# Kernel optimization log

Measured on AMD Instinct MI355X. Metric: run time of the kernel, lower is better.

Reference implementation:

```python
import jax, jax.numpy as jnp
import numpy as np
from jax import lax

NUM_KP = 17
MAX_PEOPLE = 30
HEAT_THRESH = 0.1
STRIDE = 4  # heatmap -> image coordinate scale

def setup_inputs() -> dict:
    key = jax.random.key(0)
    heatmaps = jax.random.uniform(key, (32, NUM_KP, 256, 256), dtype=jnp.float32)
    return {"heatmaps": heatmaps}

def reference(heatmaps):
    # heatmaps: [B, C, H, W]
    B, C, H, W = heatmaps.shape
    neg_inf = jnp.float32(-jnp.inf)
    # 3x3 max-pool NMS (stride 1, pad 1) batched over all B*C channels at once.
    hmax = lax.reduce_window(
        heatmaps, neg_inf, lax.max,
        window_dimensions=(1, 1, 3, 3),
        window_strides=(1, 1, 1, 1),
        padding=((0, 0), (0, 0), (1, 1), (1, 1)),
    )
    nms = heatmaps * (hmax == heatmaps).astype(heatmaps.dtype)
    # Threshold + descending sort + take top max_people, done as a batched top_k.
    flat = nms.reshape(B, C, H * W)
    masked = jnp.where(flat > HEAT_THRESH, flat, neg_inf)
    scores, idx = lax.top_k(masked, MAX_PEOPLE)          # [B, C, max_people]
    y = idx // W
    x = idx % W
    coords = jnp.stack([x, y], axis=-1).astype(jnp.int32) * STRIDE  # [B,C,max_people,2] as (x,y)*4
    valid = scores > HEAT_THRESH                          # padding mask (original output is ragged)
    return coords, scores, valid
```

## Files before the change

kernel.cpp:

```cpp
#include <hip/hip_runtime.h>
#include <stdint.h>

#define NUM_KP 17
#define BATCH  32
#define HDIM   256
#define WDIM   256
#define NCH    (BATCH * NUM_KP)
#define MAXP   30
#define QBLKS  4
#define K1THREADS 256
#define SEGCAP 640

#define NBINS  4096
#define QB     125953

#define WS_REQUIRED ((size_t)NCH * QBLKS * MAXP * 8)

__device__ __forceinline__ unsigned long long shfl_down_u64(unsigned long long v, int off) {
    unsigned lo = (unsigned)v, hi = (unsigned)(v >> 32);
    lo = __shfl_down(lo, off);
    hi = __shfl_down(hi, off);
    return ((unsigned long long)hi << 32) | lo;
}
__device__ __forceinline__ unsigned long long shfl_u64(unsigned long long v, int lane) {
    unsigned lo = (unsigned)v, hi = (unsigned)(v >> 32);
    lo = __shfl(lo, lane);
    hi = __shfl(hi, lane);
    return ((unsigned long long)hi << 32) | lo;
}
__device__ __forceinline__ unsigned quant12(float v) {
    int b = (int)(__float_as_uint(v) >> 13) - QB;
    b = b < 1 ? 1 : (b > NBINS - 1 ? NBINS - 1 : b);
    return (unsigned)b;
}

__global__ __launch_bounds__(K1THREADS, 7)
void pose_part_kernel(const float* __restrict__ heat, unsigned long long* __restrict__ part) {
    __shared__ unsigned s_buf[4 * SEGCAP];
    __shared__ unsigned s_hist[NBINS / 2];
    __shared__ int s_gsum[256];
    __shared__ unsigned long long s_ref[256];
    __shared__ int s_wcnt[4];
    __shared__ int s_nref, s_tau;

    const int tid  = threadIdx.x;
    const int chan = blockIdx.x >> 2;
    const int qtr  = blockIdx.x & 3;
    const int wave = tid >> 6;
    const int lane = tid & 63;
    const float NEGINF = -__builtin_inff();
    const float* __restrict__ cp = heat + (size_t)chan * (HDIM * WDIM);

    for (int i = tid; i < NBINS / 2; i += K1THREADS) s_hist[i] = 0;
    if (tid == 0) s_nref = 0;
    __syncthreads();

    const int r0 = (qtr << 6) + (wave << 4);
    const float* colp = cp + (lane << 2);
    const float4 NEG4 = make_float4(NEGINF, NEGINF, NEGINF, NEGINF);
    const unsigned long long ltmask = (1ull << lane) - 1ull;
    unsigned* __restrict__ seg = s_buf + wave * SEGCAP;
    int wavecnt = 0;

    auto LD = [&](int r) -> float4 {
        return (r >= 0 && r < HDIM) ? *(const float4*)(colp + (r << 8)) : NEG4;
    };
    auto push = [&](float v, int pidx, int pos) {
        if (pos < SEGCAP) {
            unsigned q = quant12(v);
            seg[pos] = (q << 16) | (unsigned)pidx;
            atomicAdd(&s_hist[q >> 1], 1u << ((q & 1) << 4));
        }
    };
    auto process = [&](const float4& up, const float4& md, const float4& dn, int r) {
        float vm0 = fmaxf(up.x, fmaxf(md.x, dn.x));
        float vm1 = fmaxf(up.y, fmaxf(md.y, dn.y));
        float vm2 = fmaxf(up.z, fmaxf(md.z, dn.z));
        float vm3 = fmaxf(up.w, fmaxf(md.w, dn.w));
        float left  = __shfl_up(vm3, 1);   if (lane == 0)  left  = NEGINF;
        float right = __shfl_down(vm0, 1); if (lane == 63) right = NEGINF;
        float h0 = fmaxf(left, fmaxf(vm0, vm1));
        float h1 = fmaxf(vm0, fmaxf(vm1, vm2));
        float h2 = fmaxf(vm1, fmaxf(vm2, vm3));
        float h3 = fmaxf(vm2, fmaxf(vm3, right));

        bool p0 = md.x > 0.1f && md.x == h0;
        bool p1 = md.y > 0.1f && md.y == h1;
        bool p2 = md.z > 0.1f && md.z == h2;
        bool p3 = md.w > 0.1f && md.w == h3;
        unsigned long long b0 = __ballot(p0), b1 = __ballot(p1);
        unsigned long long b2 = __ballot(p2), b3 = __ballot(p3);
        int c0 = __popcll(b0), c1 = __popcll(b1), c2 = __popcll(b2);
        int before = wavecnt;
        wavecnt += c0 + c1 + c2 + __popcll(b3);

        const int base = (r << 8) | (lane << 2);
        if (p0) push(md.x, base + 0, before + __popcll(b0 & ltmask));
        if (p1) push(md.y, base + 1, before + c0 + __popcll(b1 & ltmask));
        if (p2) push(md.z, base + 2, before + c0 + c1 + __popcll(b2 & ltmask));
        if (p3) push(md.w, base + 3, before + c0 + c1 + c2 + __popcll(b3 & ltmask));
    };

    float4 rm   = LD(r0 - 1);
    float4 cur0 = LD(r0 + 0), cur1 = LD(r0 + 1), cur2 = LD(r0 + 2), cur3 = LD(r0 + 3);
    #pragma unroll
    for (int g = 0; g < 4; ++g) {
        const int rb = r0 + (g << 2);
        float4 n0, n1, n2, n3;
        if (g < 3) { n0 = LD(rb + 4); n1 = LD(rb + 5); n2 = LD(rb + 6); n3 = LD(rb + 7); }
        else       { n0 = LD(rb + 4); n1 = NEG4; n2 = NEG4; n3 = NEG4; }
        process(rm,   cur0, cur1, rb + 0);
        process(cur0, cur1, cur2, rb + 1);
        process(cur1, cur2, cur3, rb + 2);
        process(cur2, cur3, n0,   rb + 3);
        rm = cur3; cur0 = n0; cur1 = n1; cur2 = n2; cur3 = n3;
    }
    if (lane == 0) s_wcnt[wave] = wavecnt < SEGCAP ? wavecnt : SEGCAP;
    __syncthreads();

    {
        int s = 0;
        #pragma unroll
        for (int j = 0; j < 8; ++j) {
            unsigned w = s_hist[tid * 8 + j];
            s += (int)(w & 0xFFFFu) + (int)(w >> 16);
        }
        s_gsum[tid] = s;
    }
    __syncthreads();
    if (wave == 0) {
        int u0 = s_gsum[(lane << 2) + 0], u1 = s_gsum[(lane << 2) + 1];
        int u2 = s_gsum[(lane << 2) + 2], u3 = s_gsum[(lane << 2) + 3];
        int t = u0 + u1 + u2 + u3;
        int R = t;
        #pragma unroll
        for (int off = 1; off < 64; off <<= 1) {
            int v = __shfl_down(R, off);
            if (lane + off < 64) R += v;
        }
        int E = R - t;
        int sg3 = u3 + E, sg2 = u2 + sg3, sg1 = u1 + sg2, sg0 = u0 + sg1;
        unsigned long long mask = __ballot(sg0 >= MAXP);
        if (mask == 0ull) {
            if (lane == 0) s_tau = 0;
        } else {
            int hi = 63 - __builtin_clzll(mask);
            if (lane == hi) {
                int k, above;
                if      (sg3 >= MAXP) { k = 3; above = E;   }
                else if (sg2 >= MAXP) { k = 2; above = sg3; }
                else if (sg1 >= MAXP) { k = 1; above = sg2; }
                else                  { k = 0; above = sg1; }
                int g = (lane << 2) + k;
                int cum = above, tau = 0;
                for (int b = (g << 4) + 15; b >= (g << 4); --b) {
                    cum += (int)((s_hist[b >> 1] >> ((b & 1) << 4)) & 0xFFFFu);
                    if (cum >= MAXP) { tau = b; break; }
                }
                s_tau = tau;
            }
        }
    }
    __syncthreads();

    const unsigned tau = (unsigned)s_tau;
    for (int s = 0; s < 4; ++s) {
        const int c = s_wcnt[s];
        const unsigned* sb = s_buf + s * SEGCAP;
        for (int i = tid; i < c; i += K1THREADS) {
            unsigned p = sb[i];
            if ((p >> 16) >= tau) {
                int pos = atomicAdd(&s_nref, 1);
                if (pos < 256) {
                    unsigned idx = p & 0xFFFFu;
                    float sc = cp[idx];
                    s_ref[pos] = ((unsigned long long)__float_as_uint(sc) << 32) | (unsigned)(~idx);
                }
            }
        }
    }
    __syncthreads();
    const int nref = s_nref < 256 ? s_nref : 256;

    if (tid < 64) {
        unsigned long long* pk = part + (size_t)blockIdx.x * MAXP;
        unsigned long long k0 = (tid       < nref) ? s_ref[tid]       : 0ull;
        unsigned long long k1 = (tid + 64  < nref) ? s_ref[tid + 64]  : 0ull;
        unsigned long long k2 = (tid + 128 < nref) ? s_ref[tid + 128] : 0ull;
        unsigned long long k3 = (tid + 192 < nref) ? s_ref[tid + 192] : 0ull;
        for (int r = 0; r < MAXP; ++r) {
            unsigned long long best = k0; int bs = 0;
            if (k1 > best) { best = k1; bs = 1; }
            if (k2 > best) { best = k2; bs = 2; }
            if (k3 > best) { best = k3; bs = 3; }
            unsigned long long key = best;
            int slot = (bs << 6) | tid;
            #pragma unroll
            for (int off = 32; off > 0; off >>= 1) {
                unsigned long long ok = shfl_down_u64(key, off);
                int os = __shfl_down(slot, off);
                if (ok > key) { key = ok; slot = os; }
            }
            key  = shfl_u64(key, 0);
            slot = __shfl(slot, 0);
            if ((slot & 63) == tid) {
                int which = slot >> 6;
                if      (which == 0) k0 = 0ull;
                else if (which == 1) k1 = 0ull;
                else if (which == 2) k2 = 0ull;
                else                 k3 = 0ull;
            }
            if (tid == 0) pk[r] = key;
        }
    }
}

__global__ __launch_bounds__(64)
void pose_merge_kernel(const unsigned long long* __restrict__ part,
                       float* __restrict__ out, int out_size) {
    const int chan = blockIdx.x;
    const int lane = threadIdx.x;
    const float NEGINF = -__builtin_inff();
    const unsigned long long* pk = part + (size_t)chan * (QBLKS * MAXP);

    unsigned long long k0 = pk[lane];
    unsigned long long k1 = (lane + 64 < QBLKS * MAXP) ? pk[lane + 64] : 0ull;

    for (int r = 0; r < MAXP; ++r) {
        unsigned long long best = k0; int bs = 0;
        if (k1 > best) { best = k1; bs = 1; }
        unsigned long long key = best;
        int slot = (bs << 6) | lane;
        #pragma unroll
        for (int off = 32; off > 0; off >>= 1) {
            unsigned long long ok = shfl_down_u64(key, off);
            int os = __shfl_down(slot, off);
            if (ok > key) { key = ok; slot = os; }
        }
        key  = shfl_u64(key, 0);
        slot = __shfl(slot, 0);
        if ((slot & 63) == lane) {
            if ((slot >> 6) == 0) k0 = 0ull; else k1 = 0ull;
        }
        if (lane == 0) {
            float sc, vld; unsigned idx;
            if (key != 0ull) {
                sc  = __uint_as_float((unsigned)(key >> 32));
                idx = (~(unsigned)key) & 0xFFFFu;
                vld = 1.0f;
            } else { sc = NEGINF; idx = 0u; vld = 0.0f; }
            int x = (int)(idx & 255), y = (int)(idx >> 8);
            long long cb = ((long long)chan * MAXP + r) * 2;
            if (cb + 1 < out_size) {
                out[cb]     = (float)(x * 4);
                out[cb + 1] = (float)(y * 4);
            }
            long long so = (long long)NCH * MAXP * 2 + (long long)chan * MAXP + r;
            if (so < out_size) out[so] = sc;
            long long vo = (long long)NCH * MAXP * 3 + (long long)chan * MAXP + r;
            if (vo < out_size) out[vo] = vld;
        }
    }
}

extern "C" void kernel_launch(void* const* d_in, const int* in_sizes, int n_in,
                              void* d_out, int out_size, void* d_ws, size_t ws_size,
                              hipStream_t stream) {
    const float* heat = (const float*)d_in[0];
    float* out = (float*)d_out;
    unsigned long long* part = (unsigned long long*)d_ws;
    hipLaunchKernelGGL(pose_part_kernel, dim3(NCH * QBLKS), dim3(K1THREADS), 0, stream,
                       heat, part);
    hipLaunchKernelGGL(pose_merge_kernel, dim3(NCH), dim3(64), 0, stream,
                       part, out, out_size);
}
```

Baseline: 237.6 us.

## Recompute NMS sweep instead of buffering candidates; rank-based top-k selection

Drops the per-wave shared-memory candidate buffer and instead re-runs the 3x3 NMS sweep a second time, emitting only candidates whose quantized score meets the threshold bin. This frees shared memory, so launch bounds are raised to eight blocks per SM. The serial 30-round wave-shuffle argmax in both kernels is replaced by parallel rank counting over shared memory, and the merge kernel uses 128 threads. The cost is a second read of the heatmap tile (likely served from cache) and the NMS arithmetic done twice.

Result: slower. 394.2 us (+65.9%).

```diff
diff --git a/kernel.cpp b/kernel.cpp
--- a/kernel.cpp
+++ b/kernel.cpp
@@ -9,38 +9,23 @@
 #define MAXP   30
 #define QBLKS  4
 #define K1THREADS 256
-#define SEGCAP 640
 
 #define NBINS  4096
 #define QB     125953
 
 #define WS_REQUIRED ((size_t)NCH * QBLKS * MAXP * 8)
 
-__device__ __forceinline__ unsigned long long shfl_down_u64(unsigned long long v, int off) {
-    unsigned lo = (unsigned)v, hi = (unsigned)(v >> 32);
-    lo = __shfl_down(lo, off);
-    hi = __shfl_down(hi, off);
-    return ((unsigned long long)hi << 32) | lo;
-}
-__device__ __forceinline__ unsigned long long shfl_u64(unsigned long long v, int lane) {
-    unsigned lo = (unsigned)v, hi = (unsigned)(v >> 32);
-    lo = __shfl(lo, lane);
-    hi = __shfl(hi, lane);
-    return ((unsigned long long)hi << 32) | lo;
-}
 __device__ __forceinline__ unsigned quant12(float v) {
     int b = (int)(__float_as_uint(v) >> 13) - QB;
     b = b < 1 ? 1 : (b > NBINS - 1 ? NBINS - 1 : b);
     return (unsigned)b;
 }
 
-__global__ __launch_bounds__(K1THREADS, 7)
+__global__ __launch_bounds__(K1THREADS, 8)
 void pose_part_kernel(const float* __restrict__ heat, unsigned long long* __restrict__ part) {
-    __shared__ unsigned s_buf[4 * SEGCAP];
     __shared__ unsigned s_hist[NBINS / 2];
     __shared__ int s_gsum[256];
     __shared__ unsigned long long s_ref[256];
-    __shared__ int s_wcnt[4];
     __shared__ int s_nref, s_tau;
 
     const int tid  = threadIdx.x;
@@ -58,21 +43,12 @@
     const int r0 = (qtr << 6) + (wave << 4);
     const float* colp = cp + (lane << 2);
     const float4 NEG4 = make_float4(NEGINF, NEGINF, NEGINF, NEGINF);
-    const unsigned long long ltmask = (1ull << lane) - 1ull;
-    unsigned* __restrict__ seg = s_buf + wave * SEGCAP;
-    int wavecnt = 0;
 
     auto LD = [&](int r) -> float4 {
         return (r >= 0 && r < HDIM) ? *(const float4*)(colp + (r << 8)) : NEG4;
     };
-    auto push = [&](float v, int pidx, int pos) {
-        if (pos < SEGCAP) {
-            unsigned q = quant12(v);
-            seg[pos] = (q << 16) | (unsigned)pidx;
-            atomicAdd(&s_hist[q >> 1], 1u << ((q & 1) << 4));
-        }
-    };
-    auto process = [&](const float4& up, const float4& md, const float4& dn, int r) {
+    auto process = [&](const float4& up, const float4& md, const float4& dn, int r,
+                       auto&& emit) {
         float vm0 = fmaxf(up.x, fmaxf(md.x, dn.x));
         float vm1 = fmaxf(up.y, fmaxf(md.y, dn.y));
         float vm2 = fmaxf(up.z, fmaxf(md.z, dn.z));
@@ -83,39 +59,34 @@
         float h1 = fmaxf(vm0, fmaxf(vm1, vm2));
         float h2 = fmaxf(vm1, fmaxf(vm2, vm3));
         float h3 = fmaxf(vm2, fmaxf(vm3, right));
-
-        bool p0 = md.x > 0.1f && md.x == h0;
-        bool p1 = md.y > 0.1f && md.y == h1;
-        bool p2 = md.z > 0.1f && md.z == h2;
-        bool p3 = md.w > 0.1f && md.w == h3;
-        unsigned long long b0 = __ballot(p0), b1 = __ballot(p1);
-        unsigned long long b2 = __ballot(p2), b3 = __ballot(p3);
-        int c0 = __popcll(b0), c1 = __popcll(b1), c2 = __popcll(b2);
-        int before = wavecnt;
-        wavecnt += c0 + c1 + c2 + __popcll(b3);
-
         const int base = (r << 8) | (lane << 2);
-        if (p0) push(md.x, base + 0, before + __popcll(b0 & ltmask));
-        if (p1) push(md.y, base + 1, before + c0 + __popcll(b1 & ltmask));
-        if (p2) push(md.z, base + 2, before + c0 + c1 + __popcll(b2 & ltmask));
-        if (p3) push(md.w, base + 3, before + c0 + c1 + c2 + __popcll(b3 & ltmask));
+        if (md.x > 0.1f && md.x == h0) emit(md.x, base + 0);
+        if (md.y > 0.1f && md.y == h1) emit(md.y, base + 1);
+        if (md.z > 0.1f && md.z == h2) emit(md.z, base + 2);
+        if (md.w > 0.1f && md.w == h3) emit(md.w, base + 3);
     };
-
-    float4 rm   = LD(r0 - 1);
-    float4 cur0 = LD(r0 + 0), cur1 = LD(r0 + 1), cur2 = LD(r0 + 2), cur3 = LD(r0 + 3);
-    #pragma unroll
-    for (int g = 0; g < 4; ++g) {
-        const int rb = r0 + (g << 2);
-        float4 n0, n1, n2, n3;
-        if (g < 3) { n0 = LD(rb + 4); n1 = LD(rb + 5); n2 = LD(rb + 6); n3 = LD(rb + 7); }
-        else       { n0 = LD(rb + 4); n1 = NEG4; n2 = NEG4; n3 = NEG4; }
-        process(rm,   cur0, cur1, rb + 0);
-        process(cur0, cur1, cur2, rb + 1);
-        process(cur1, cur2, cur3, rb + 2);
-        process(cur2, cur3, n0,   rb + 3);
-        rm = cur3; cur0 = n0; cur1 = n1; cur2 = n2; cur3 = n3;
-    }
-    if (lane == 0) s_wcnt[wave] = wavecnt < SEGCAP ? wavecnt : SEGCAP;
+    auto sweep = [&](auto&& emit) {
+        float4 rm   = LD(r0 - 1);
+        float4 cur0 = LD(r0 + 0), cur1 = LD(r0 + 1), cur2 = LD(r0 + 2), cur3 = LD(r0 + 3);
+        #pragma unroll
+        for (int g = 0; g < 4; ++g) {
+            const int rb = r0 + (g << 2);
+            float4 n0, n1, n2, n3;
+            if (g < 3) { n0 = LD(rb + 4); n1 = LD(rb + 5); n2 = LD(rb + 6); n3 = LD(rb + 7); }
+            else       { n0 = LD(rb + 4); n1 = NEG4; n2 = NEG4; n3 = NEG4; }
+            process(rm,   cur0, cur1, rb + 0, emit);
+            process(cur0, cur1, cur2, rb + 1, emit);
+            process(cur1, cur2, cur3, rb + 2, emit);
+            process(cur2, cur3, n0,   rb + 3, emit);
+            rm = cur3; cur0 = n0; cur1 = n1; cur2 = n2; cur3 = n3;
+        }
+    };
+
+    sweep([&](float v, int pidx) {
+        unsigned q = quant12(v);
+        atomicAdd(&s_hist[q >> 1], 1u << ((q & 1) << 4));
+        (void)pidx;
+    });
     __syncthreads();
 
     {
@@ -164,100 +135,65 @@
     __syncthreads();
 
     const unsigned tau = (unsigned)s_tau;
-    for (int s = 0; s < 4; ++s) {
-        const int c = s_wcnt[s];
-        const unsigned* sb = s_buf + s * SEGCAP;
-        for (int i = tid; i < c; i += K1THREADS) {
-            unsigned p = sb[i];
-            if ((p >> 16) >= tau) {
-                int pos = atomicAdd(&s_nref, 1);
-                if (pos < 256) {
-                    unsigned idx = p & 0xFFFFu;
-                    float sc = cp[idx];
-                    s_ref[pos] = ((unsigned long long)__float_as_uint(sc) << 32) | (unsigned)(~idx);
-                }
+    sweep([&](float v, int pidx) {
+        if (quant12(v) >= tau) {
+            int pos = atomicAdd(&s_nref, 1);
+            if (pos < 256) {
+                s_ref[pos] = ((unsigned long long)__float_as_uint(v) << 32)
+                           | (unsigned)(~(unsigned)pidx);
             }
         }
-    }
-    __syncthreads();
+    });
+    __syncthreads();
+
     const int nref = s_nref < 256 ? s_nref : 256;
-
-    if (tid < 64) {
-        unsigned long long* pk = part + (size_t)blockIdx.x * MAXP;
-        unsigned long long k0 = (tid       < nref) ? s_ref[tid]       : 0ull;
-        unsigned long long k1 = (tid + 64  < nref) ? s_ref[tid + 64]  : 0ull;
-        unsigned long long k2 = (tid + 128 < nref) ? s_ref[tid + 128] : 0ull;
-        unsigned long long k3 = (tid + 192 < nref) ? s_ref[tid + 192] : 0ull;
-        for (int r = 0; r < MAXP; ++r) {
-            unsigned long long best = k0; int bs = 0;
-            if (k1 > best) { best = k1; bs = 1; }
-            if (k2 > best) { best = k2; bs = 2; }
-            if (k3 > best) { best = k3; bs = 3; }
-            unsigned long long key = best;
-            int slot = (bs << 6) | tid;
-            #pragma unroll
-            for (int off = 32; off > 0; off >>= 1) {
-                unsigned long long ok = shfl_down_u64(key, off);
-                int os = __shfl_down(slot, off);
-                if (ok > key) { key = ok; slot = os; }
-            }
-            key  = shfl_u64(key, 0);
-            slot = __shfl(slot, 0);
-            if ((slot & 63) == tid) {
-                int which = slot >> 6;
-                if      (which == 0) k0 = 0ull;
-                else if (which == 1) k1 = 0ull;
-                else if (which == 2) k2 = 0ull;
-                else                 k3 = 0ull;
-            }
-            if (tid == 0) pk[r] = key;
-        }
-    }
-}
-
-__global__ __launch_bounds__(64)
+    unsigned long long* pk = part + (size_t)blockIdx.x * MAXP;
+    const int nv = nref < MAXP ? nref : MAXP;
+    if (tid >= nv && tid < MAXP) pk[tid] = 0ull;
+    if (tid < nref) {
+        unsigned long long k = s_ref[tid];
+        int rank = 0;
+        for (int j = 0; j < nref; ++j) rank += (s_ref[j] > k) ? 1 : 0;
+        if (rank < MAXP) pk[rank] = k;
+    }
+}
+
+__global__ __launch_bounds__(128)
 void pose_merge_kernel(const unsigned long long* __restrict__ part,
                        float* __restrict__ out, int out_size) {
+    __shared__ unsigned long long s_k[128];
     const int chan = blockIdx.x;
-    const int lane = threadIdx.x;
+    const int tid  = threadIdx.x;
+    const int NK   = QBLKS * MAXP;
     const float NEGINF = -__builtin_inff();
-    const unsigned long long* pk = part + (size_t)chan * (QBLKS * MAXP);
-
-    unsigned long long k0 = pk[lane];
-    unsigned long long k1 = (lane + 64 < QBLKS * MAXP) ? pk[lane + 64] : 0ull;
-
-    for (int r = 0; r < MAXP; ++r) {
-        unsigned long long best = k0; int bs = 0;
-        if (k1 > best) { best = k1; bs = 1; }
-        unsigned long long key = best;
-        int slot = (bs << 6) | lane;
-        #pragma unroll
-        for (int off = 32; off > 0; off >>= 1) {
-            unsigned long long ok = shfl_down_u64(key, off);
-            int os = __shfl_down(slot, off);
-            if (ok > key) { key = ok; slot = os; }
-        }
-        key  = shfl_u64(key, 0);
-        slot = __shfl(slot, 0);
-        if ((slot & 63) == lane) {
-            if ((slot >> 6) == 0) k0 = 0ull; else k1 = 0ull;
-        }
-        if (lane == 0) {
+    const unsigned long long* pk = part + (size_t)chan * NK;
+
+    s_k[tid] = (tid < NK) ? pk[tid] : 0ull;
+    __syncthreads();
+
+    if (tid < NK) {
+        unsigned long long k = s_k[tid];
+        int rank = 0;
+        for (int j = 0; j < NK; ++j) {
+            unsigned long long o = s_k[j];
+            rank += (o > k || (o == k && j < tid)) ? 1 : 0;
+        }
+        if (rank < MAXP) {
             float sc, vld; unsigned idx;
-            if (key != 0ull) {
-                sc  = __uint_as_float((unsigned)(key >> 32));
-                idx = (~(unsigned)key) & 0xFFFFu;
+            if (k != 0ull) {
+                sc  = __uint_as_float((unsigned)(k >> 32));
+                idx = (~(unsigned)k) & 0xFFFFu;
                 vld = 1.0f;
             } else { sc = NEGINF; idx = 0u; vld = 0.0f; }
             int x = (int)(idx & 255), y = (int)(idx >> 8);
-            long long cb = ((long long)chan * MAXP + r) * 2;
+            long long cb = ((long long)chan * MAXP + rank) * 2;
             if (cb + 1 < out_size) {
                 out[cb]     = (float)(x * 4);
                 out[cb + 1] = (float)(y * 4);
             }
-            long long so = (long long)NCH * MAXP * 2 + (long long)chan * MAXP + r;
+            long long so = (long long)NCH * MAXP * 2 + (long long)chan * MAXP + rank;
             if (so < out_size) out[so] = sc;
-            long long vo = (long long)NCH * MAXP * 3 + (long long)chan * MAXP + r;
+            long long vo = (long long)NCH * MAXP * 3 + (long long)chan * MAXP + rank;
             if (vo < out_size) out[vo] = vld;
         }
     }
@@ -271,6 +207,6 @@
     unsigned long long* part = (unsigned long long*)d_ws;
     hipLaunchKernelGGL(pose_part_kernel, dim3(NCH * QBLKS), dim3(K1THREADS), 0, stream,
                        heat, part);
-    hipLaunchKernelGGL(pose_merge_kernel, dim3(NCH), dim3(64), 0, stream,
+    hipLaunchKernelGGL(pose_merge_kernel, dim3(NCH), dim3(128), 0, stream,
                        part, out, out_size);
 }
```
